# Kernel tuning notes

Hardware: AMD Instinct MI355X
Metric: run time of the kernel (lower is better)

Reference implementation:

```python
import jax, jax.numpy as jnp
import numpy as np

ALPHA = 0.2  # LeakyReLU negative slope
NEG_INF = -1e12


def setup_inputs() -> dict:
    key = jax.random.key(0)
    k1, k2, k3, k4 = jax.random.split(key, 4)
    B, N, F_in, F_out = 8, 4096, 128, 64
    inp = jax.random.normal(k1, (B, N, F_in), dtype=jnp.float32)
    adj = jax.random.randint(k2, (B, N, N), 0, 2, dtype=jnp.int32)
    # xavier-uniform-ish init for W, a
    W = jax.random.normal(k3, (F_in, F_out), dtype=jnp.float32) * (2.0 / (F_in + F_out)) ** 0.5
    a = jax.random.normal(k4, (2 * F_out, 1), dtype=jnp.float32) * (2.0 / (2 * F_out + 1)) ** 0.5
    return {"inp": inp, "adj": adj, "W": W, "a": a}


def reference(inp, adj, W, a):
    # inp: [B,N,F_in], adj: [B,N,N] int, W: [F_in,F_out], a: [2*F_out,1]
    F_out = W.shape[1]
    h = jnp.einsum('bnf,fo->bno', inp, W)          # [B,N,F_out]
    a1 = a[:F_out, 0]                              # [F_out]
    a2 = a[F_out:, 0]                              # [F_out]
    # e[b,i,j] = leakyrelu(h_i . a1 + h_j . a2)  (== concat([h_i,h_j]) @ a)
    s1 = h @ a1                                    # [B,N]
    s2 = h @ a2                                    # [B,N]
    e = s1[:, :, None] + s2[:, None, :]            # [B,N,N]
    e = jnp.where(e > 0, e, ALPHA * e)             # LeakyReLU
    att = jnp.where(adj > 0, e, NEG_INF)
    att = jax.nn.softmax(att, axis=-1)             # [B,N,N]
    # dropout p=0.0 -> identity
    h_prime = jnp.einsum('bij,bjo->bio', att, h)   # [B,N,F_out]
    return jax.nn.elu(h_prime)
```

## Files before the change

kernel.cpp:

```cpp
#include <hip/hip_runtime.h>
#include <hip/hip_bf16.h>
#include <hip/hip_fp16.h>
#include <cstdint>

typedef __attribute__((ext_vector_type(8))) short short8;
typedef __attribute__((ext_vector_type(4))) float floatx4;

#define LEAKY_ALPHA 0.2f

__device__ __forceinline__ unsigned short f2bf_rne(float f) {
    unsigned u = __float_as_uint(f);
    unsigned r = u + 0x7FFFu + ((u >> 16) & 1u);
    return (unsigned short)(r >> 16);
}

__device__ __forceinline__ unsigned pk2bf(float lo, float hi) {
    union { __hip_bfloat162 b; unsigned u; } c;
    c.b = __float22bfloat162_rn(make_float2(lo, hi));
    return c.u;
}

__device__ __forceinline__ float2 h2f2(unsigned w) {
    union { unsigned u; __half2 h; } c; c.u = w;
    return __half22float2(c.h);
}

__global__ __launch_bounds__(256) void k_h(const float* __restrict__ inp,
                                           const float* __restrict__ W,
                                           const float* __restrict__ a,
                                           unsigned short* __restrict__ hT,
                                           float2* __restrict__ e1,
                                           __half2* __restrict__ e2h) {
    __shared__ float hs[64][65];
    const int tid  = threadIdx.x;
    const int wv   = tid >> 6;
    const int lane = tid & 63;
    const int blk  = blockIdx.x;
    const int b     = blk >> 6;
    const int ibase = (blk & 63) * 64;

    const float a1 = a[lane];
    const float a2 = a[64 + lane];

    for (int rr = 0; rr < 16; ++rr) {
        const int rloc = wv * 16 + rr;
        const int row  = ibase + rloc;
        const float* ip = inp + ((size_t)(b * 4096 + row)) * 128;
        float acc = 0.f;
        #pragma unroll
        for (int f = 0; f < 128; f += 4) {
            float4 v = *(const float4*)(ip + f);
            acc += v.x * W[(f + 0) * 64 + lane];
            acc += v.y * W[(f + 1) * 64 + lane];
            acc += v.z * W[(f + 2) * 64 + lane];
            acc += v.w * W[(f + 3) * 64 + lane];
        }
        hs[rloc][lane] = acc;
        float r1 = acc * a1;
        float r2 = acc * a2;
        #pragma unroll
        for (int off = 32; off > 0; off >>= 1) {
            r1 += __shfl_xor(r1, off);
            r2 += __shfl_xor(r2, off);
        }
        if (lane == 0) {
            e1[b * 4096 + row]  = make_float2(__expf(r1), __expf(LEAKY_ALPHA * r1));
            e2h[b * 4096 + row] = __floats2half2_rn(__expf(r2), __expf(LEAKY_ALPHA * r2));
        }
    }
    __syncthreads();

    const int o    = tid & 63;
    const int half = tid >> 6;
    const int tl   = half >> 1;
    const int nco  = (half & 1) * 16;
    unsigned pk[8];
    #pragma unroll
    for (int s = 0; s < 16; s += 2) {
        unsigned lo = f2bf_rne(hs[tl * 32 + nco + s    ][o]);
        unsigned hi = f2bf_rne(hs[tl * 32 + nco + s + 1][o]);
        pk[s >> 1] = lo | (hi << 16);
    }
    const int tile = (ibase >> 5) + tl;
    unsigned short* dst = hT + (((size_t)b * 128 + tile) * 64 + o) * 32 + nco;
    *(int4*)(dst)     = *(int4*)&pk[0];
    *(int4*)(dst + 8) = *(int4*)&pk[4];
}

__global__ __launch_bounds__(256, 4) void k_fused(const int* __restrict__ adj,
                                                  const unsigned short* __restrict__ hT,
                                                  const float2* __restrict__ e1g,
                                                  const __half2* __restrict__ e2hg,
                                                  float* __restrict__ out) {
    __shared__ unsigned maskw[32][129];
    __shared__ __half2 e2s[4096];

    const int tid   = threadIdx.x;
    const int b     = blockIdx.x >> 7;
    const int rtile = blockIdx.x & 127;
    const int wv    = tid >> 6;
    const int lane  = tid & 63;

    {
        const __half2* src = e2hg + b * 4096;
        #pragma unroll
        for (int t = 0; t < 4; ++t) {
            int idx = tid * 16 + t * 4;
            *(int4*)&e2s[idx] = *(const int4*)(src + idx);
        }
    }

    {
        const int* abase = adj + ((size_t)(b * 4096 + rtile * 32)) * 4096
                         + (size_t)wv * 32768;
        #pragma unroll 2
        for (int i = 0; i < 16; ++i) {
            const int* p = abase + i * 2048 + lane * 32;
            unsigned w = 0;
            #pragma unroll
            for (int k = 0; k < 8; ++k) {
                const int4 v = *(const int4*)(p + k * 4);
                w |= (v.x > 0 ? 1u : 0u) << (k * 4 + 0);
                w |= (v.y > 0 ? 1u : 0u) << (k * 4 + 1);
                w |= (v.z > 0 ? 1u : 0u) << (k * 4 + 2);
                w |= (v.w > 0 ? 1u : 0u) << (k * 4 + 3);
            }
            maskw[wv * 8 + (i >> 1)][(i & 1) * 64 + lane] = w;
        }
    }
    __syncthreads();

    const int jhalf = wv >> 1;
    const int m     = lane & 15;
    const int kh    = lane >> 4;
    const int rl    = (wv & 1) * 16 + m;
    const int rbase = rtile * 32 + (wv & 1) * 16;
    const int row   = rbase + m;

    const float2 E1 = e1g[b * 4096 + row];
    const float E1p = E1.x, E1n = E1.y;
    const int jb0 = jhalf * 2048 + kh * 8;
    const unsigned* mrow = &maskw[rl][jhalf * 64];

    const unsigned short* hbase =
        hT + (((size_t)b * 128 + jhalf * 64) * 64 + m) * 32 + kh * 8;
    const unsigned short* hrow0 = hbase;
    const unsigned short* hrow1 = hbase + 512;
    const unsigned short* hrow2 = hbase + 1024;
    const unsigned short* hrow3 = hbase + 1536;

    floatx4 acc0 = (floatx4){0.f,0.f,0.f,0.f};
    floatx4 acc1 = (floatx4){0.f,0.f,0.f,0.f};
    floatx4 acc2 = (floatx4){0.f,0.f,0.f,0.f};
    floatx4 acc3 = (floatx4){0.f,0.f,0.f,0.f};
    float lsum = 0.f;

    unsigned rm_0, rm_1;
    short8 rb0_0, rb1_0, rb2_0, rb3_0, rb0_1, rb1_1, rb2_1, rb3_1;

    rm_0  = mrow[0];
    rb0_0 = *(const short8*)(hrow0);         rb1_0 = *(const short8*)(hrow1);
    rb2_0 = *(const short8*)(hrow2);         rb3_0 = *(const short8*)(hrow3);
    rm_1  = mrow[1];
    rb0_1 = *(const short8*)(hrow0 + 2048);  rb1_1 = *(const short8*)(hrow1 + 2048);
    rb2_1 = *(const short8*)(hrow2 + 2048);  rb3_1 = *(const short8*)(hrow3 + 2048);

#define GAT_COL(WRD, T)                                                        \
    {                                                                          \
        const float2 ef = h2f2((unsigned)(WRD));                               \
        const float P  = E1p * ef.x;                                           \
        const float Nn = E1n * ef.y;                                           \
        float p = (P > 1.0f) ? P : Nn;                                         \
        p = ((mb >> (T)) & 1u) ? p : 0.0f;                                     \
        psum += p;                                                             \
        pv[T] = p;                                                             \
    }

#define GAT_STEP(SL, STEPIDX)                                                  \
    do {                                                                       \
        const unsigned cmw = rm_##SL;                                          \
        const short8 cb0 = rb0_##SL, cb1 = rb1_##SL;                           \
        const short8 cb2 = rb2_##SL, cb3 = rb3_##SL;                           \
        const int pstep = ((STEPIDX) + 2) & 63;         \
        const int poff = pstep * 2048;                         \
        rm_##SL  = mrow[pstep];                                                \
        rb0_##SL = *(const short8*)(hrow0 + poff);                             \
        rb1_##SL = *(const short8*)(hrow1 + poff);                             \
        rb2_##SL = *(const short8*)(hrow2 + poff);                             \
        rb3_##SL = *(const short8*)(hrow3 + poff);                             \
        const int soff = jb0 + (STEPIDX) * 32;                                 \
        const int4 eA = *(const int4*)&e2s[soff];                              \
        const int4 eB = *(const int4*)&e2s[soff + 4];                          \
        const unsigned mb = (cmw >> (kh * 8)) & 0xffu;                         \
        float pv[8];                                                           \
        float psum = 0.f;                                                      \
        GAT_COL(eA.x, 0) GAT_COL(eA.y, 1) GAT_COL(eA.z, 2) GAT_COL(eA.w, 3)    \
        GAT_COL(eB.x, 4) GAT_COL(eB.y, 5) GAT_COL(eB.z, 6) GAT_COL(eB.w, 7)    \
        lsum += psum;                                                          \
        int4 ai;                                                               \
        ai.x = pk2bf(pv[0], pv[1]); ai.y = pk2bf(pv[2], pv[3]);                \
        ai.z = pk2bf(pv[4], pv[5]); ai.w = pk2bf(pv[6], pv[7]);                \
        union { int4 i; short8 s; } cc; cc.i = ai;                             \
        const short8 af = cc.s;                                                \
        acc0 = __builtin_amdgcn_mfma_f32_16x16x32_bf16(af, cb0, acc0, 0,0,0);  \
        acc1 = __builtin_amdgcn_mfma_f32_16x16x32_bf16(af, cb1, acc1, 0,0,0);  \
        acc2 = __builtin_amdgcn_mfma_f32_16x16x32_bf16(af, cb2, acc2, 0,0,0);  \
        acc3 = __builtin_amdgcn_mfma_f32_16x16x32_bf16(af, cb3, acc3, 0,0,0);  \
    } while (0)

    #pragma unroll 1
    for (int it = 0; it < 32; ++it) {
        const int s0 = it * 2;
        GAT_STEP(0, s0);
        GAT_STEP(1, s0 + 1);
    }
#undef GAT_STEP
#undef GAT_COL

    lsum += __shfl_xor(lsum, 16);
    lsum += __shfl_xor(lsum, 32);

    floatx4 accs[4] = {acc0, acc1, acc2, acc3};

    float* accb = (float*)&maskw[0][0];
    float* lb   = accb + 2 * 64 * 17;

    __syncthreads();
    if (wv >= 2) {
        #pragma unroll
        for (int f = 0; f < 4; ++f)
            #pragma unroll
            for (int r = 0; r < 4; ++r)
                accb[(wv - 2) * 64 * 17 + lane * 17 + f * 4 + r] = accs[f][r];
        lb[(wv - 2) * 64 + lane] = lsum;
    }
    __syncthreads();
    if (wv < 2) {
        const float ltot = lsum + lb[wv * 64 + lane];
        #pragma unroll
        for (int f = 0; f < 4; ++f) {
            #pragma unroll
            for (int r = 0; r < 4; ++r) {
                float v = accs[f][r] + accb[wv * 64 * 17 + lane * 17 + f * 4 + r];
                const int drow = (lane >> 4) * 4 + r;
                const float lr = __shfl(ltot, drow);
                const float hp = v / lr;
                const float o  = (hp > 0.f) ? hp : (__expf(hp) - 1.f);
                out[((size_t)(b * 4096 + rbase + drow)) * 64 + f * 16 + (lane & 15)] = o;
            }
        }
    }
}

extern "C" void kernel_launch(void* const* d_in, const int* in_sizes, int n_in,
                              void* d_out, int out_size, void* d_ws, size_t ws_size,
                              hipStream_t stream) {
    const float* inp = (const float*)d_in[0];
    const int*   adj = (const int*)d_in[1];
    const float* W   = (const float*)d_in[2];
    const float* a   = (const float*)d_in[3];
    float* out = (float*)d_out;

    unsigned short* hT = (unsigned short*)d_ws;
    float2*  e1  = (float2*)((char*)d_ws + (size_t)4 * 1024 * 1024);
    __half2* e2h = (__half2*)((char*)d_ws + (size_t)4 * 1024 * 1024 + 262144);

    k_h<<<512, 256, 0, stream>>>(inp, W, a, hT, e1, e2h);
    k_fused<<<1024, 256, 0, stream>>>(adj, hT, e1, e2h, out);
}
```

Measured before the change: 815.6 us.

## Interleave ballot-based adjacency mask packing with the attention MFMA loop

The adjacency-to-bitmask conversion now uses wave ballots instead of per-lane bit shifting, and it runs in chunks interleaved with the main gather/MFMA loop rather than as a full prologue. The goal is to overlap the large adj global reads with compute. To match the ballot bit order, the column order inside each 32-wide tile of hT and e2 is permuted. This adds a block-wide barrier per chunk and more shared-memory stores by lane 0.

```diff
diff --git a/kernel.cpp b/kernel.cpp
--- a/kernel.cpp
+++ b/kernel.cpp
@@ -24,6 +24,7 @@
     union { unsigned u; __half2 h; } c; c.u = w;
     return __half22float2(c.h);
 }
+
 
 __global__ __launch_bounds__(256) void k_h(const float* __restrict__ inp,
                                            const float* __restrict__ W,
@@ -77,8 +78,11 @@
     unsigned pk[8];
     #pragma unroll
     for (int s = 0; s < 16; s += 2) {
-        unsigned lo = f2bf_rne(hs[tl * 32 + nco + s    ][o]);
-        unsigned hi = f2bf_rne(hs[tl * 32 + nco + s + 1][o]);
+        const int n0 = nco + s, n1 = nco + s + 1;
+        const int c0 = 4 * (n0 & 7) + (n0 >> 3);
+        const int c1 = 4 * (n1 & 7) + (n1 >> 3);
+        unsigned lo = f2bf_rne(hs[tl * 32 + c0][o]);
+        unsigned hi = f2bf_rne(hs[tl * 32 + c1][o]);
         pk[s >> 1] = lo | (hi << 16);
     }
     const int tile = (ibase >> 5) + tl;
@@ -92,8 +96,8 @@
                                                   const float2* __restrict__ e1g,
                                                   const __half2* __restrict__ e2hg,
                                                   float* __restrict__ out) {
-    __shared__ unsigned maskw[32][129];
-    __shared__ __half2 e2s[4096];
+    __shared__ unsigned long long mask64[32][17][4];
+    __shared__ unsigned e2su[4096];
 
     const int tid   = threadIdx.x;
     const int b     = blockIdx.x >> 7;
@@ -102,33 +106,46 @@
     const int lane  = tid & 63;
 
     {
-        const __half2* src = e2hg + b * 4096;
+        const unsigned* src = (const unsigned*)(e2hg + b * 4096);
         #pragma unroll
         for (int t = 0; t < 4; ++t) {
-            int idx = tid * 16 + t * 4;
-            *(int4*)&e2s[idx] = *(const int4*)(src + idx);
-        }
-    }
-
-    {
-        const int* abase = adj + ((size_t)(b * 4096 + rtile * 32)) * 4096
-                         + (size_t)wv * 32768;
-        #pragma unroll 2
-        for (int i = 0; i < 16; ++i) {
-            const int* p = abase + i * 2048 + lane * 32;
-            unsigned w = 0;
-            #pragma unroll
-            for (int k = 0; k < 8; ++k) {
-                const int4 v = *(const int4*)(p + k * 4);
-                w |= (v.x > 0 ? 1u : 0u) << (k * 4 + 0);
-                w |= (v.y > 0 ? 1u : 0u) << (k * 4 + 1);
-                w |= (v.z > 0 ? 1u : 0u) << (k * 4 + 2);
-                w |= (v.w > 0 ? 1u : 0u) << (k * 4 + 3);
-            }
-            maskw[wv * 8 + (i >> 1)][(i & 1) * 64 + lane] = w;
-        }
-    }
-    __syncthreads();
+            const int c0 = tid * 16 + t * 4;
+            const int4 raw = *(const int4*)(src + c0);
+            const int base = (c0 & ~31) + ((c0 & 31) >> 2);
+            e2su[base +  0] = (unsigned)raw.x;
+            e2su[base +  8] = (unsigned)raw.y;
+            e2su[base + 16] = (unsigned)raw.z;
+            e2su[base + 24] = (unsigned)raw.w;
+        }
+    }
+
+    const int* abase = adj + ((size_t)(b * 4096 + rtile * 32)) * 4096;
+
+#define PACK_ONE(LR, GRP)                                                      \
+    {                                                                          \
+        const int4 v = *(const int4*)(abase + (size_t)(LR) * 4096              \
+                                      + (GRP) * 256 + lane * 4);               \
+        const unsigned long long b0 = __ballot(v.x > 0);                       \
+        const unsigned long long b1 = __ballot(v.y > 0);                       \
+        const unsigned long long b2 = __ballot(v.z > 0);                       \
+        const unsigned long long b3 = __ballot(v.w > 0);                       \
+        if (lane == 0) {                                                       \
+            ulonglong2* d = (ulonglong2*)&mask64[LR][GRP][0];                  \
+            ulonglong2 t0; t0.x = b0; t0.y = b1;                               \
+            ulonglong2 t1; t1.x = b2; t1.y = b3;                               \
+            d[0] = t0; d[1] = t1;                                              \
+        }                                                                      \
+    }
+
+#define PACK2(GA, GB)                                                          \
+    _Pragma("unroll 2")                                                        \
+    for (int r = 0; r < 8; ++r) {                                              \
+        const int lr = wv * 8 + r;                                             \
+        PACK_ONE(lr, (GA));                                                    \
+        PACK_ONE(lr, (GB));                                                    \
+    }
+
+    PACK2(0, 8);
 
     const int jhalf = wv >> 1;
     const int m     = lane & 15;
@@ -140,7 +157,6 @@
     const float2 E1 = e1g[b * 4096 + row];
     const float E1p = E1.x, E1n = E1.y;
     const int jb0 = jhalf * 2048 + kh * 8;
-    const unsigned* mrow = &maskw[rl][jhalf * 64];
 
     const unsigned short* hbase =
         hT + (((size_t)b * 128 + jhalf * 64) * 64 + m) * 32 + kh * 8;
@@ -155,15 +171,13 @@
     floatx4 acc3 = (floatx4){0.f,0.f,0.f,0.f};
     float lsum = 0.f;
 
-    unsigned rm_0, rm_1;
     short8 rb0_0, rb1_0, rb2_0, rb3_0, rb0_1, rb1_1, rb2_1, rb3_1;
-
-    rm_0  = mrow[0];
     rb0_0 = *(const short8*)(hrow0);         rb1_0 = *(const short8*)(hrow1);
     rb2_0 = *(const short8*)(hrow2);         rb3_0 = *(const short8*)(hrow3);
-    rm_1  = mrow[1];
     rb0_1 = *(const short8*)(hrow0 + 2048);  rb1_1 = *(const short8*)(hrow1 + 2048);
     rb2_1 = *(const short8*)(hrow2 + 2048);  rb3_1 = *(const short8*)(hrow3 + 2048);
+
+    __syncthreads();
 
 #define GAT_COL(WRD, T)                                                        \
     {                                                                          \
@@ -178,20 +192,18 @@
 
 #define GAT_STEP(SL, STEPIDX)                                                  \
     do {                                                                       \
-        const unsigned cmw = rm_##SL;                                          \
         const short8 cb0 = rb0_##SL, cb1 = rb1_##SL;                           \
         const short8 cb2 = rb2_##SL, cb3 = rb3_##SL;                           \
         const int pstep = ((STEPIDX) + 2) & 63;         \
         const int poff = pstep * 2048;                         \
-        rm_##SL  = mrow[pstep];                                                \
         rb0_##SL = *(const short8*)(hrow0 + poff);                             \
         rb1_##SL = *(const short8*)(hrow1 + poff);                             \
         rb2_##SL = *(const short8*)(hrow2 + poff);                             \
         rb3_##SL = *(const short8*)(hrow3 + poff);                             \
         const int soff = jb0 + (STEPIDX) * 32;                                 \
-        const int4 eA = *(const int4*)&e2s[soff];                              \
-        const int4 eB = *(const int4*)&e2s[soff + 4];                          \
-        const unsigned mb = (cmw >> (kh * 8)) & 0xffu;                         \
+        const int4 eA = *(const int4*)&e2su[soff];                             \
+        const int4 eB = *(const int4*)&e2su[soff + 4];                         \
+        const unsigned mb = (unsigned)(Mcur >> (8 * ((STEPIDX) & 7))) & 0xffu; \
         float pv[8];                                                           \
         float psum = 0.f;                                                      \
         GAT_COL(eA.x, 0) GAT_COL(eA.y, 1) GAT_COL(eA.z, 2) GAT_COL(eA.w, 3)    \
@@ -209,23 +221,32 @@
     } while (0)
 
     #pragma unroll 1
-    for (int it = 0; it < 32; ++it) {
-        const int s0 = it * 2;
-        GAT_STEP(0, s0);
-        GAT_STEP(1, s0 + 1);
+    for (int p = 0; p < 8; ++p) {
+        const unsigned long long Mcur =
+            *(const unsigned long long*)&mask64[rl][jhalf * 8 + p][kh];
+        #pragma unroll
+        for (int q = 0; q < 4; ++q) {
+            GAT_STEP(0, p * 8 + 2 * q);
+            GAT_STEP(1, p * 8 + 2 * q + 1);
+        }
+        if (p < 7) {
+            PACK2(p + 1, p + 9);
+        }
+        __syncthreads();
     }
 #undef GAT_STEP
 #undef GAT_COL
+#undef PACK2
+#undef PACK_ONE
 
     lsum += __shfl_xor(lsum, 16);
     lsum += __shfl_xor(lsum, 32);
 
     floatx4 accs[4] = {acc0, acc1, acc2, acc3};
 
-    float* accb = (float*)&maskw[0][0];
+    float* accb = (float*)&mask64[0][0][0];
     float* lb   = accb + 2 * 64 * 17;
 
-    __syncthreads();
     if (wv >= 2) {
         #pragma unroll
         for (int f = 0; f < 4; ++f)
```

Measured after the change: 902.1 us. 10.6% more time.

## Split adjacency bitmask packing into a separate streaming kernel

Applied to the files above, without the earlier changes.

Adds a k_pack kernel that streams the int32 adjacency matrix with nontemporal loads and writes a compact 1-bit-per-edge mask to workspace. The attention kernel now loads a small precomputed mask tile instead of reading and packing adjacency in its prologue. This aims to give the bandwidth-bound adjacency read full occupancy, separate from the MFMA-heavy kernel's limited occupancy. It costs an extra launch and a write and read of the mask.

```diff
diff --git a/kernel.cpp b/kernel.cpp
--- a/kernel.cpp
+++ b/kernel.cpp
@@ -5,6 +5,7 @@
 
 typedef __attribute__((ext_vector_type(8))) short short8;
 typedef __attribute__((ext_vector_type(4))) float floatx4;
+typedef __attribute__((ext_vector_type(4))) int   intx4;
 
 #define LEAKY_ALPHA 0.2f
 
@@ -23,6 +24,22 @@
 __device__ __forceinline__ float2 h2f2(unsigned w) {
     union { unsigned u; __half2 h; } c; c.u = w;
     return __half22float2(c.h);
+}
+
+__global__ __launch_bounds__(256) void k_pack(const int* __restrict__ adj,
+                                              unsigned* __restrict__ mask) {
+    const size_t t = (size_t)blockIdx.x * 256 + threadIdx.x;
+    const int* p = adj + t * 32;
+    unsigned m = 0;
+    #pragma unroll
+    for (int k = 0; k < 8; ++k) {
+        const intx4 v = __builtin_nontemporal_load((const intx4*)(p + k * 4));
+        m |= (v.x > 0 ? 1u : 0u) << (k * 4 + 0);
+        m |= (v.y > 0 ? 1u : 0u) << (k * 4 + 1);
+        m |= (v.z > 0 ? 1u : 0u) << (k * 4 + 2);
+        m |= (v.w > 0 ? 1u : 0u) << (k * 4 + 3);
+    }
+    mask[t] = m;
 }
 
 __global__ __launch_bounds__(256) void k_h(const float* __restrict__ inp,
@@ -87,13 +104,13 @@
     *(int4*)(dst + 8) = *(int4*)&pk[4];
 }
 
-__global__ __launch_bounds__(256, 4) void k_fused(const int* __restrict__ adj,
-                                                  const unsigned short* __restrict__ hT,
-                                                  const float2* __restrict__ e1g,
-                                                  const __half2* __restrict__ e2hg,
-                                                  float* __restrict__ out) {
-    __shared__ unsigned maskw[32][129];
-    __shared__ __half2 e2s[4096];
+__global__ __launch_bounds__(256, 4) void k_attn(const unsigned* __restrict__ mask,
+                                                 const unsigned short* __restrict__ hT,
+                                                 const float2* __restrict__ e1g,
+                                                 const __half2* __restrict__ e2hg,
+                                                 float* __restrict__ out) {
+    __shared__ unsigned maskl[32][132];
+    __shared__ unsigned e2su[4096];
 
     const int tid   = threadIdx.x;
     const int b     = blockIdx.x >> 7;
@@ -102,30 +119,20 @@
     const int lane  = tid & 63;
 
     {
-        const __half2* src = e2hg + b * 4096;
+        const unsigned* src = (const unsigned*)(e2hg + b * 4096);
         #pragma unroll
         for (int t = 0; t < 4; ++t) {
             int idx = tid * 16 + t * 4;
-            *(int4*)&e2s[idx] = *(const int4*)(src + idx);
-        }
-    }
-
+            *(int4*)&e2su[idx] = *(const int4*)(src + idx);
+        }
+    }
     {
-        const int* abase = adj + ((size_t)(b * 4096 + rtile * 32)) * 4096
-                         + (size_t)wv * 32768;
-        #pragma unroll 2
-        for (int i = 0; i < 16; ++i) {
-            const int* p = abase + i * 2048 + lane * 32;
-            unsigned w = 0;
-            #pragma unroll
-            for (int k = 0; k < 8; ++k) {
-                const int4 v = *(const int4*)(p + k * 4);
-                w |= (v.x > 0 ? 1u : 0u) << (k * 4 + 0);
-                w |= (v.y > 0 ? 1u : 0u) << (k * 4 + 1);
-                w |= (v.z > 0 ? 1u : 0u) << (k * 4 + 2);
-                w |= (v.w > 0 ? 1u : 0u) << (k * 4 + 3);
-            }
-            maskw[wv * 8 + (i >> 1)][(i & 1) * 64 + lane] = w;
+        const unsigned* gm = mask + ((size_t)(b * 4096 + rtile * 32)) * 128;
+        #pragma unroll
+        for (int q = 0; q < 4; ++q) {
+            const int f = tid * 16 + q * 4;
+            const intx4 v = __builtin_nontemporal_load((const intx4*)(gm + f));
+            *(intx4*)&maskl[f >> 7][f & 127] = v;
         }
     }
     __syncthreads();
@@ -140,7 +147,7 @@
     const float2 E1 = e1g[b * 4096 + row];
     const float E1p = E1.x, E1n = E1.y;
     const int jb0 = jhalf * 2048 + kh * 8;
-    const unsigned* mrow = &maskw[rl][jhalf * 64];
+    const unsigned* mrow = &maskl[rl][jhalf * 64];
 
     const unsigned short* hbase =
         hT + (((size_t)b * 128 + jhalf * 64) * 64 + m) * 32 + kh * 8;
@@ -189,8 +196,8 @@
         rb2_##SL = *(const short8*)(hrow2 + poff);                             \
         rb3_##SL = *(const short8*)(hrow3 + poff);                             \
         const int soff = jb0 + (STEPIDX) * 32;                                 \
-        const int4 eA = *(const int4*)&e2s[soff];                              \
-        const int4 eB = *(const int4*)&e2s[soff + 4];                          \
+        const int4 eA = *(const int4*)&e2su[soff];                             \
+        const int4 eB = *(const int4*)&e2su[soff + 4];                         \
         const unsigned mb = (cmw >> (kh * 8)) & 0xffu;                         \
         float pv[8];                                                           \
         float psum = 0.f;                                                      \
@@ -222,7 +229,7 @@
 
     floatx4 accs[4] = {acc0, acc1, acc2, acc3};
 
-    float* accb = (float*)&maskw[0][0];
+    float* accb = (float*)&maskl[0][0];
     float* lb   = accb + 2 * 64 * 17;
 
     __syncthreads();
@@ -262,9 +269,11 @@
     float* out = (float*)d_out;
 
     unsigned short* hT = (unsigned short*)d_ws;
-    float2*  e1  = (float2*)((char*)d_ws + (size_t)4 * 1024 * 1024);
-    __half2* e2h = (__half2*)((char*)d_ws + (size_t)4 * 1024 * 1024 + 262144);
-
+    float2*  e1   = (float2*)((char*)d_ws + (size_t)4 * 1024 * 1024);
+    __half2* e2h  = (__half2*)((char*)d_ws + (size_t)4 * 1024 * 1024 + 262144);
+    unsigned* mask = (unsigned*)((char*)d_ws + (size_t)6 * 1024 * 1024);
+
+    k_pack<<<16384, 256, 0, stream>>>(adj, mask);
     k_h<<<512, 256, 0, stream>>>(inp, W, a, hT, e1, e2h);
-    k_fused<<<1024, 256, 0, stream>>>(adj, hT, e1, e2h, out);
-}
+    k_attn<<<1024, 256, 0, stream>>>(mask, hT, e1, e2h, out);
+}
```

Result: slower. 918.3 us (+12.6%).
